# Optimization experiments

Measured on AMD Instinct MI355X. Metric: run time of the kernel, lower is better.

Reference implementation:

```python
import jax, jax.numpy as jnp
import numpy as np

N, E, DIN, HID, DOUT = 50000, 800000, 128, 128, 64
NEG_SLOPE = 0.2


def setup_inputs() -> dict:
    key = jax.random.key(0)
    ks = jax.random.split(key, 16)
    x = jax.random.normal(ks[0], (N, DIN), dtype=jnp.float32)
    edge_index = jax.random.randint(ks[1], (2, E), 0, N, dtype=jnp.int64)

    def lin(k, fan_in, fan_out):
        kw, kb = jax.random.split(k)
        s = 1.0 / np.sqrt(fan_in)
        W = jax.random.uniform(kw, (fan_in, fan_out), jnp.float32, -s, s)
        b = jax.random.uniform(kb, (fan_out,), jnp.float32, -s, s)
        return W, b

    Wl, bl = lin(ks[2], DIN, DIN)   # GATv2 lin_l
    Wr, br = lin(ks[3], DIN, DIN)   # GATv2 lin_r
    att = jax.random.uniform(ks[4], (DIN,), jnp.float32, -1.0 / np.sqrt(DIN), 1.0 / np.sqrt(DIN))
    bg = jnp.zeros((DIN,), jnp.float32)  # GAT output bias
    W1, b1 = lin(ks[5], DIN, HID)   # ChebConv K=1 -> plain linear
    W2, b2 = lin(ks[6], HID, HID)
    W3, b3 = lin(ks[7], HID, DOUT)
    return {"x": x, "edge_index": edge_index, "Wl": Wl, "bl": bl, "Wr": Wr,
            "br": br, "att": att, "bg": bg, "W1": W1, "b1": b1,
            "W2": W2, "b2": b2, "W3": W3, "b3": b3}


def reference(x, edge_index, Wl, bl, Wr, br, att, bg, W1, b1, W2, b2, W3, b3):
    n = x.shape[0]
    # GATv2Conv adds self loops by default
    loop = jnp.arange(n, dtype=edge_index.dtype)
    src = jnp.concatenate([edge_index[0], loop])  # source j
    dst = jnp.concatenate([edge_index[1], loop])  # target i

    xl = x @ Wl + bl  # [N, DIN]
    xr = x @ Wr + br  # [N, DIN]

    # GATv2 edge scores: leaky_relu(x_l[j] + x_r[i]) . att
    e = jax.nn.leaky_relu(xl[src] + xr[dst], NEG_SLOPE)  # [E+N, DIN]
    a = e @ att                                          # [E+N]

    # softmax over incoming edges of each destination node
    amax = jax.ops.segment_max(a, dst, num_segments=n)
    ea = jnp.exp(a - amax[dst])
    denom = jax.ops.segment_sum(ea, dst, num_segments=n)
    alpha = ea / denom[dst]                              # [E+N]

    # aggregate messages alpha * x_l[j] at destinations
    h = jax.ops.segment_sum(alpha[:, None] * xl[src], dst, num_segments=n) + bg

    # ChebConv with K=1 reduces to a linear layer (T_0(L) = I)
    h = jax.nn.relu(h @ W1 + b1)
    h = jax.nn.relu(h @ W2 + b2)
    # dropout_rate = 0.0 -> identity
    return h @ W3 + b3
```

## Files before the change

### kernel.cpp

```cpp
#include <hip/hip_runtime.h>
#include <hip/hip_bf16.h>

#define DIN 128
#define NEG_SLOPE 0.2f
#define PTILE 4096
#define PAD 64
#define SPAD 4608
#define CVT_BLKS 289

typedef __attribute__((ext_vector_type(8))) short bf16x8;
typedef __attribute__((ext_vector_type(8))) unsigned short u16x8;
typedef __attribute__((ext_vector_type(4))) float f32x4;
typedef __attribute__((ext_vector_type(2))) float f32x2;
typedef __attribute__((ext_vector_type(4))) unsigned int u32x4;

__device__ __forceinline__ ushort f2bf(float f) {
  unsigned u = __float_as_uint(f);
  u += 0x7FFFu + ((u >> 16) & 1u);
  return (ushort)(u >> 16);
}
__device__ __forceinline__ f32x2 bfpair(unsigned u) {
  f32x2 r;
  r.x = __uint_as_float(u << 16);
  r.y = __uint_as_float(u & 0xFFFF0000u);
  return r;
}

template <int CTRL>
__device__ __forceinline__ float dppadd(float x) {
  int v = __builtin_amdgcn_update_dpp(0, __float_as_int(x), CTRL, 0xf, 0xf, true);
  return x + __int_as_float(v);
}
__device__ __forceinline__ float red16(float t) {
  t = dppadd<0xB1>(t);
  t = dppadd<0x4E>(t);
  t = dppadd<0x141>(t);
  t = dppadd<0x140>(t);
  return t;
}

__global__ __launch_bounds__(256) void part_cvt_kernel(
    const int* __restrict__ ei, unsigned* __restrict__ part,
    int* __restrict__ cnt2, int ntile, int E,
    const float* __restrict__ Wl, const float* __restrict__ Wr,
    const float* __restrict__ W1, const float* __restrict__ W2,
    const float* __restrict__ W3,
    ushort* __restrict__ WlT, ushort* __restrict__ WrT,
    ushort* __restrict__ W1T, ushort* __restrict__ W2T,
    ushort* __restrict__ W3T) {
  if ((int)blockIdx.x < ntile) {
    __shared__ int hist[256], pref[256], sexcl[256], curs[256];
    __shared__ unsigned buf[PTILE];
    const int tid = threadIdx.x;
    const int t = blockIdx.x;
    const int tile0 = t * PTILE;
    const int tcount = min(PTILE, E - tile0);
    hist[tid] = 0;
    __syncthreads();
    unsigned pk[PTILE / 256];
    int cnt = 0;
    for (int i = tid; i < tcount; i += 256) {
      int s = ei[tile0 + i], d = ei[E + tile0 + i];
      unsigned p = ((unsigned)d << 16) | (unsigned)s;
      pk[cnt++] = p;
      atomicAdd(&hist[d >> 8], 1);
    }
    __syncthreads();
    int v = hist[tid];
    pref[tid] = v;
    __syncthreads();
    for (int d = 1; d < 256; d <<= 1) {
      int tt = (tid >= d) ? pref[tid - d] : 0;
      __syncthreads();
      pref[tid] += tt;
      __syncthreads();
    }
    int exc = pref[tid] - v;
    sexcl[tid] = exc;
    curs[tid] = exc;
    cnt2[tid * ntile + t] = v;
    __syncthreads();
    for (int j = 0; j < cnt; j++) {
      int b = pk[j] >> 24;
      int pos = atomicAdd(&curs[b], 1);
      buf[pos] = pk[j];
    }
    __syncthreads();
    for (int i = tid; i < tcount; i += 256) {
      unsigned p = buf[i];
      int b = p >> 24;
      int r = i - sexcl[b];
      if (r < PAD)
        part[((long)b * ntile + t) * PAD + r] = p;
    }
  } else {
    int i = ((int)blockIdx.x - ntile) * 256 + threadIdx.x;
    if (i < 16384) {
      int k = i >> 7, c = i & 127; WlT[c * 128 + k] = f2bf(Wl[i]);
    } else if (i < 32768) {
      int j = i - 16384; int k = j >> 7, c = j & 127; WrT[c * 128 + k] = f2bf(Wr[j]);
    } else if (i < 49152) {
      int j = i - 32768; int k = j >> 7, c = j & 127; W1T[c * 128 + k] = f2bf(W1[j]);
    } else if (i < 65536) {
      int j = i - 49152; int k = j >> 7, c = j & 127; W2T[c * 128 + k] = f2bf(W2[j]);
    } else if (i < 73728) {
      int j = i - 65536; int k = j >> 6, c = j & 63; W3T[c * 128 + k] = f2bf(W3[j]);
    }
  }
}

__global__ __launch_bounds__(1024) void lin_fine_kernel(
    const float* __restrict__ x,
    const ushort* __restrict__ WlT, const float* __restrict__ bl,
    const ushort* __restrict__ WrT, const float* __restrict__ br,
    ushort* __restrict__ xl, ushort* __restrict__ xr, int n, int nblk_gemm,
    const unsigned* __restrict__ part, const int* __restrict__ cnt2,
    int* __restrict__ offsets, ushort* __restrict__ ecnt,
    ushort* __restrict__ ssrc, int ntile, int N) {
  if ((int)blockIdx.x < nblk_gemm) {
    const int tid1 = threadIdx.x;
    const int sub = tid1 >> 8, tid = tid1 & 255;
    const int wv = tid >> 6, lane = tid & 63;
    const int m = lane & 15, quad = lane >> 4;
    const int colbase = (wv & 1) * 64;
    const int nodew = blockIdx.x * 128 + sub * 32 + (wv >> 1) * 16;
    int arow = nodew + m; if (arow >= n) arow = n - 1;
    f32x4 accl[4], accr[4];
#pragma unroll
    for (int nt = 0; nt < 4; nt++) { accl[nt] = (f32x4){0,0,0,0}; accr[nt] = (f32x4){0,0,0,0}; }
#pragma unroll
    for (int kk = 0; kk < 4; kk++) {
      int k0 = kk * 32 + quad * 8;
      const float4* xp = (const float4*)(x + (long)arow * 128 + k0);
      float4 x0 = xp[0], x1 = xp[1];
      bf16x8 af;
      af[0] = (short)f2bf(x0.x); af[1] = (short)f2bf(x0.y);
      af[2] = (short)f2bf(x0.z); af[3] = (short)f2bf(x0.w);
      af[4] = (short)f2bf(x1.x); af[5] = (short)f2bf(x1.y);
      af[6] = (short)f2bf(x1.z); af[7] = (short)f2bf(x1.w);
#pragma unroll
      for (int nt = 0; nt < 4; nt++) {
        int brow = colbase + nt * 16 + m;
        bf16x8 bl8 = *(const bf16x8*)(WlT + brow * 128 + k0);
        bf16x8 br8 = *(const bf16x8*)(WrT + brow * 128 + k0);
        accl[nt] = __builtin_amdgcn_mfma_f32_16x16x32_bf16(af, bl8, accl[nt], 0, 0, 0);
        accr[nt] = __builtin_amdgcn_mfma_f32_16x16x32_bf16(af, br8, accr[nt], 0, 0, 0);
      }
    }
#pragma unroll
    for (int nt = 0; nt < 4; nt++) {
      int col = colbase + nt * 16 + m;
      float vbl = bl[col], vbr = br[col];
#pragma unroll
      for (int r = 0; r < 4; r++) {
        int node = nodew + quad * 4 + r;
        if (node < n) {
          xl[(long)node * 128 + col] = f2bf(accl[nt][r] + vbl);
          xr[(long)node * 128 + col] = f2bf(accr[nt][r] + vbr);
        }
      }
    }
  } else {
    __shared__ int cnt2s[256], hist[256], curs[256];
    const int tid = threadIdx.x;
    const int b = (int)blockIdx.x - nblk_gemm;
    if (tid < 256) {
      hist[tid] = 0;
      cnt2s[tid] = (tid < ntile) ? cnt2[b * ntile + tid] : 0;
    }
    __syncthreads();
    const long base = (long)b * ntile * PAD;
    const int nv = ntile * PAD;
    for (int v = tid; v < nv; v += 1024) {
      int t = v >> 6;
      if ((v & 63) < cnt2s[t]) {
        unsigned p = part[base + v];
        atomicAdd(&hist[(p >> 16) & 255], 1);
      }
    }
    __syncthreads();
    int v0 = (tid < 256) ? hist[tid] : 0;
    if (tid < 256) curs[tid] = v0;
    __syncthreads();
    for (int d = 1; d < 256; d <<= 1) {
      int tt = (tid >= d && tid < 256) ? curs[tid - d] : 0;
      __syncthreads();
      if (tid < 256) curs[tid] += tt;
      __syncthreads();
    }
    if (tid < 256) {
      int excl = curs[tid] - v0;
      int node = b * 256 + tid;
      if (node < N) {
        offsets[node] = b * SPAD + excl;
        ecnt[node] = (ushort)v0;
      }
      curs[tid] = b * SPAD + excl;
    }
    __syncthreads();
    for (int v = tid; v < nv; v += 1024) {
      int t = v >> 6;
      if ((v & 63) < cnt2s[t]) {
        unsigned p = part[base + v];
        int pos = atomicAdd(&curs[(p >> 16) & 255], 1);
        ssrc[pos] = (ushort)(p & 0xFFFFu);
      }
    }
  }
}

__global__ __launch_bounds__(256) void node_aggr_kernel(
    const ushort* __restrict__ xl, const ushort* __restrict__ xr,
    const float* __restrict__ att, const float* __restrict__ bg,
    const int* __restrict__ offsets, const ushort* __restrict__ ecnt,
    const ushort* __restrict__ ssrc, ushort* __restrict__ h, int n) {
  int wave = (int)((blockIdx.x * (long)blockDim.x + threadIdx.x) >> 6);
  int lane = threadIdx.x & 63;
  if (wave >= n) return;
  const int node = wave;
  const int eg = lane >> 4, sl = lane & 15;
  const int beg = offsets[node];
  const int end = beg + (int)ecnt[node];
  const int last = end - 1;
  const ushort* __restrict__ xls = xl + sl * 8;
  int ia0 = beg + 2 * eg;
  int sa  = (int)ssrc[min(ia0, last)];
  int sb  = (int)ssrc[min(ia0 + 1, last)];
  int sa2 = (int)ssrc[min(ia0 + 8, last)];
  int sb2 = (int)ssrc[min(ia0 + 9, last)];
  u32x4 uva = *(const u32x4*)(xls + (long)sa * 128);
  u32x4 uvb = *(const u32x4*)(xls + (long)sb * 128);

  f32x2 a06[4], a04[4], r2[4], acc2[4];
  {
    const float4* ap = (const float4*)(att + sl * 8);
    float4 a0 = ap[0], a1 = ap[1];
    f32x2 av[4] = {{a0.x, a0.y}, {a0.z, a0.w}, {a1.x, a1.y}, {a1.z, a1.w}};
#pragma unroll
    for (int jp = 0; jp < 4; jp++) {
      a06[jp] = 0.6f * av[jp];
      a04[jp] = 0.4f * av[jp];
    }
  }
  u32x4 rv = *(const u32x4*)(xr + (long)node * 128 + sl * 8);
  u32x4 lv = *(const u32x4*)(xls + (long)node * 128);
  float denom;
  {
    f32x2 t1 = {0.f, 0.f}, t2 = {0.f, 0.f};
    f32x2 l2[4];
#pragma unroll
    for (int jp = 0; jp < 4; jp++) {
      r2[jp] = bfpair(rv[jp]);
      l2[jp] = bfpair(lv[jp]);
      f32x2 v = l2[jp] + r2[jp];
      t1 += a06[jp] * v;
      t2 += a04[jp] * __builtin_elementwise_abs(v);
    }
    float t = red16(t1.x + t1.y + t2.x + t2.y);
    float es = __expf(t);
    denom = (eg == 0) ? es : 0.f;
#pragma unroll
    for (int jp = 0; jp < 4; jp++)
      acc2[jp] = (eg == 0) ? es * l2[jp] : (f32x2){0.f, 0.f};
  }
  for (int p = beg; p < end; p += 8) {
    u32x4 ca = uva, cb = uvb;
    int ia = p + 2 * eg;
    bool cva = ia < end, cvb = ia + 1 < end;
    uva = *(const u32x4*)(xls + (long)sa2 * 128);
    uvb = *(const u32x4*)(xls + (long)sb2 * 128);
    int ian = p + 16 + 2 * eg;
    sa2 = (int)ssrc[min(ian, last)];
    sb2 = (int)ssrc[min(ian + 1, last)];
    f32x2 ua2[4], ub2[4];
    f32x2 ta1 = {0.f, 0.f}, ta2 = {0.f, 0.f};
    f32x2 tb1 = {0.f, 0.f}, tb2 = {0.f, 0.f};
#pragma unroll
    for (int jp = 0; jp < 4; jp++) {
      ua2[jp] = bfpair(ca[jp]);
      ub2[jp] = bfpair(cb[jp]);
      f32x2 va2 = ua2[jp] + r2[jp];
      f32x2 vb2 = ub2[jp] + r2[jp];
      ta1 += a06[jp] * va2;
      ta2 += a04[jp] * __builtin_elementwise_abs(va2);
      tb1 += a06[jp] * vb2;
      tb2 += a04[jp] * __builtin_elementwise_abs(vb2);
    }
    float ta = red16(ta1.x + ta1.y + ta2.x + ta2.y);
    float tb = red16(tb1.x + tb1.y + tb2.x + tb2.y);
    float ea = cva ? __expf(ta) : 0.f;
    float eb = cvb ? __expf(tb) : 0.f;
    denom += ea + eb;
#pragma unroll
    for (int jp = 0; jp < 4; jp++)
      acc2[jp] += ea * ua2[jp] + eb * ub2[jp];
  }
#pragma unroll
  for (int jp = 0; jp < 4; jp++) {
    acc2[jp].x += __shfl_xor(acc2[jp].x, 16);
    acc2[jp].y += __shfl_xor(acc2[jp].y, 16);
    acc2[jp].x += __shfl_xor(acc2[jp].x, 32);
    acc2[jp].y += __shfl_xor(acc2[jp].y, 32);
  }
  denom += __shfl_xor(denom, 16);
  denom += __shfl_xor(denom, 32);
  if (eg == 0) {
    float inv = 1.0f / denom;
    const float4* bp = (const float4*)(bg + sl * 8);
    float4 g0 = bp[0], g1 = bp[1];
    f32x2 gv[4] = {{g0.x, g0.y}, {g0.z, g0.w}, {g1.x, g1.y}, {g1.z, g1.w}};
    u16x8 o;
#pragma unroll
    for (int jp = 0; jp < 4; jp++) {
      f32x2 hv = acc2[jp] * inv + gv[jp];
      o[2 * jp]     = f2bf(hv.x);
      o[2 * jp + 1] = f2bf(hv.y);
    }
    *(u16x8*)(h + (long)node * 128 + sl * 8) = o;
  }
}

#define LDSP 136
__global__ __launch_bounds__(256) void mlp_mfma_kernel(
    const ushort* __restrict__ hb,
    const ushort* __restrict__ W1T, const float* __restrict__ b1,
    const ushort* __restrict__ W2T, const float* __restrict__ b2,
    const ushort* __restrict__ W3T, const float* __restrict__ b3,
    float* __restrict__ out, int n) {
  __shared__ ushort act[32][LDSP];
  const int tid = threadIdx.x;
  const int wv = tid >> 6, lane = tid & 63;
  const int m = lane & 15, quad = lane >> 4;
  const int half = wv & 1, ng = wv >> 1;
  const int colbase = half * 64;
  const int nodew = blockIdx.x * 32 + ng * 16;
  int arow = nodew + m; if (arow >= n) arow = n - 1;
  f32x4 acc[4];
#pragma unroll
  for (int nt = 0; nt < 4; nt++) acc[nt] = (f32x4){0,0,0,0};
#pragma unroll
  for (int kk = 0; kk < 4; kk++) {
    int k0 = kk * 32 + quad * 8;
    bf16x8 af = *(const bf16x8*)(hb + (long)arow * 128 + k0);
#pragma unroll
    for (int nt = 0; nt < 4; nt++) {
      bf16x8 b8 = *(const bf16x8*)(W1T + (colbase + nt * 16 + m) * 128 + k0);
      acc[nt] = __builtin_amdgcn_mfma_f32_16x16x32_bf16(af, b8, acc[nt], 0, 0, 0);
    }
  }
#pragma unroll
  for (int nt = 0; nt < 4; nt++) {
    int col = colbase + nt * 16 + m;
    float b = b1[col];
#pragma unroll
    for (int r = 0; r < 4; r++)
      act[ng * 16 + quad * 4 + r][col] = f2bf(fmaxf(acc[nt][r] + b, 0.f));
  }
  __syncthreads();
#pragma unroll
  for (int nt = 0; nt < 4; nt++) acc[nt] = (f32x4){0,0,0,0};
#pragma unroll
  for (int kk = 0; kk < 4; kk++) {
    int k0 = kk * 32 + quad * 8;
    bf16x8 af = *(const bf16x8*)(&act[ng * 16 + m][k0]);
#pragma unroll
    for (int nt = 0; nt < 4; nt++) {
      bf16x8 b8 = *(const bf16x8*)(W2T + (colbase + nt * 16 + m) * 128 + k0);
      acc[nt] = __builtin_amdgcn_mfma_f32_16x16x32_bf16(af, b8, acc[nt], 0, 0, 0);
    }
  }
  __syncthreads();
#pragma unroll
  for (int nt = 0; nt < 4; nt++) {
    int col = colbase + nt * 16 + m;
    float b = b2[col];
#pragma unroll
    for (int r = 0; r < 4; r++)
      act[ng * 16 + quad * 4 + r][col] = f2bf(fmaxf(acc[nt][r] + b, 0.f));
  }
  __syncthreads();
  f32x4 acc3[2];
#pragma unroll
  for (int nt = 0; nt < 2; nt++) acc3[nt] = (f32x4){0,0,0,0};
#pragma unroll
  for (int kk = 0; kk < 4; kk++) {
    int k0 = kk * 32 + quad * 8;
    bf16x8 af = *(const bf16x8*)(&act[ng * 16 + m][k0]);
#pragma unroll
    for (int nt = 0; nt < 2; nt++) {
      bf16x8 b8 = *(const bf16x8*)(W3T + (half * 32 + nt * 16 + m) * 128 + k0);
      acc3[nt] = __builtin_amdgcn_mfma_f32_16x16x32_bf16(af, b8, acc3[nt], 0, 0, 0);
    }
  }
#pragma unroll
  for (int nt = 0; nt < 2; nt++) {
    int col = half * 32 + nt * 16 + m;
    float b = b3[col];
#pragma unroll
    for (int r = 0; r < 4; r++) {
      int node = nodew + quad * 4 + r;
      if (node < n) out[(long)node * 64 + col] = acc3[nt][r] + b;
    }
  }
}

extern "C" void kernel_launch(void* const* d_in, const int* in_sizes, int n_in,
                              void* d_out, int out_size, void* d_ws, size_t ws_size,
                              hipStream_t stream) {
  const float* x   = (const float*)d_in[0];
  const int*   ei  = (const int*)d_in[1];
  const float* Wl  = (const float*)d_in[2];
  const float* bl  = (const float*)d_in[3];
  const float* Wr  = (const float*)d_in[4];
  const float* br  = (const float*)d_in[5];
  const float* att = (const float*)d_in[6];
  const float* bg  = (const float*)d_in[7];
  const float* W1  = (const float*)d_in[8];
  const float* b1  = (const float*)d_in[9];
  const float* W2  = (const float*)d_in[10];
  const float* b2  = (const float*)d_in[11];
  const float* W3  = (const float*)d_in[12];
  const float* b3  = (const float*)d_in[13];
  float* out = (float*)d_out;

  const int N = in_sizes[0] / DIN;
  const int E = in_sizes[1] / 2;
  const int nbuck = (N + 255) >> 8;
  const int ntile = (E + PTILE - 1) / PTILE;

  char* ws = (char*)d_ws;
  size_t off = 0;
  auto alloc = [&](size_t bytes) {
    void* p = ws + off;
    off += (bytes + 255) & ~(size_t)255;
    return p;
  };
  int* cnt2      = (int*)alloc((size_t)256 * ntile * 4);
  int* offsets   = (int*)alloc(((size_t)N + 4) * 4);
  ushort* ecnt   = (ushort*)alloc(((size_t)N + 16) * 2);
  ushort* ssrc   = (ushort*)alloc((size_t)256 * SPAD * 2 + 256);
  ushort* xlb    = (ushort*)alloc((size_t)N * DIN * 2);
  ushort* xrb    = (ushort*)alloc((size_t)N * DIN * 2);
  size_t part_bytes = (size_t)256 * ntile * PAD * 4;
  size_t hbf_bytes  = (size_t)N * DIN * 2;
  unsigned* part = (unsigned*)alloc(part_bytes > hbf_bytes ? part_bytes : hbf_bytes);
  ushort* hbf    = (ushort*)part;
  ushort* WlT    = (ushort*)alloc(16384 * 2);
  ushort* WrT    = (ushort*)alloc(16384 * 2);
  ushort* W1T    = (ushort*)alloc(16384 * 2);
  ushort* W2T    = (ushort*)alloc(16384 * 2);
  ushort* W3T    = (ushort*)alloc(8192 * 2);
  (void)ws_size;

  part_cvt_kernel<<<ntile + CVT_BLKS, 256, 0, stream>>>(
      ei, part, cnt2, ntile, E,
      Wl, Wr, W1, W2, W3, WlT, WrT, W1T, W2T, W3T);

  int nblk_gemm = (N + 127) / 128;
  lin_fine_kernel<<<nblk_gemm + nbuck, 1024, 0, stream>>>(
      x, WlT, bl, WrT, br, xlb, xrb, N, nblk_gemm,
      part, cnt2, offsets, ecnt, ssrc, ntile, N);

  int nwblk = (N + 3) / 4;
  node_aggr_kernel<<<nwblk, 256, 0, stream>>>(xlb, xrb, att, bg,
                                              offsets, ecnt, ssrc, hbf, N);

  int nblk32 = (N + 31) / 32;
  mlp_mfma_kernel<<<nblk32, 256, 0, stream>>>(hbf, W1T, b1, W2T, b2,
                                              W3T, b3, out, N);
}
```

Before: 237.6 us.

## Precompute per-node attention dot products and stage GEMM tiles through LDS

Splits leaky_relu as 0.6*v + 0.4*|v|, so the linear term's dot with att becomes per-node scalars al and ar. These are computed in the GEMM epilogue and added per edge, removing half the per-edge FMA work in aggregation at the cost of one extra scalar load per edge. The GEMM now stages the bf16 x tile and the outputs through shared memory for coalesced 16-byte loads and stores, and the MLP kernel stages its h input tile in LDS as well. These add synchronisation barriers and LDS usage.

```diff
diff --git a/kernel.cpp b/kernel.cpp
--- a/kernel.cpp
+++ b/kernel.cpp
@@ -18,6 +18,9 @@
   unsigned u = __float_as_uint(f);
   u += 0x7FFFu + ((u >> 16) & 1u);
   return (ushort)(u >> 16);
+}
+__device__ __forceinline__ float bf2f(ushort u) {
+  return __uint_as_float((unsigned)u << 16);
 }
 __device__ __forceinline__ f32x2 bfpair(unsigned u) {
   f32x2 r;
@@ -109,35 +112,46 @@
   }
 }
 
+#define XSP 136
 __global__ __launch_bounds__(1024) void lin_fine_kernel(
-    const float* __restrict__ x,
+    const float* __restrict__ x, const float* __restrict__ att,
     const ushort* __restrict__ WlT, const float* __restrict__ bl,
     const ushort* __restrict__ WrT, const float* __restrict__ br,
-    ushort* __restrict__ xl, ushort* __restrict__ xr, int n, int nblk_gemm,
+    ushort* __restrict__ xl, ushort* __restrict__ xr,
+    float* __restrict__ al, float* __restrict__ ar, int n, int nblk_gemm,
     const unsigned* __restrict__ part, const int* __restrict__ cnt2,
     int* __restrict__ offsets, ushort* __restrict__ ecnt,
     ushort* __restrict__ ssrc, int ntile, int N) {
   if ((int)blockIdx.x < nblk_gemm) {
+    __shared__ ushort xs[4][32][XSP];
     const int tid1 = threadIdx.x;
     const int sub = tid1 >> 8, tid = tid1 & 255;
     const int wv = tid >> 6, lane = tid & 63;
     const int m = lane & 15, quad = lane >> 4;
     const int colbase = (wv & 1) * 64;
-    const int nodew = blockIdx.x * 128 + sub * 32 + (wv >> 1) * 16;
-    int arow = nodew + m; if (arow >= n) arow = n - 1;
+    const int ng = wv >> 1;
+    const int nodew0 = blockIdx.x * 128 + sub * 32;
+    const int srow = tid >> 3, scol = (tid & 7) * 16;
+    {
+      int grow = nodew0 + srow; if (grow >= n) grow = n - 1;
+      const float4* xp = (const float4*)(x + (long)grow * 128 + scol);
+      float4 f0 = xp[0], f1 = xp[1], f2 = xp[2], f3 = xp[3];
+      u16x8 o0, o1;
+      o0[0] = f2bf(f0.x); o0[1] = f2bf(f0.y); o0[2] = f2bf(f0.z); o0[3] = f2bf(f0.w);
+      o0[4] = f2bf(f1.x); o0[5] = f2bf(f1.y); o0[6] = f2bf(f1.z); o0[7] = f2bf(f1.w);
+      o1[0] = f2bf(f2.x); o1[1] = f2bf(f2.y); o1[2] = f2bf(f2.z); o1[3] = f2bf(f2.w);
+      o1[4] = f2bf(f3.x); o1[5] = f2bf(f3.y); o1[6] = f2bf(f3.z); o1[7] = f2bf(f3.w);
+      *(u16x8*)&xs[sub][srow][scol]     = o0;
+      *(u16x8*)&xs[sub][srow][scol + 8] = o1;
+    }
+    __syncthreads();
     f32x4 accl[4], accr[4];
 #pragma unroll
     for (int nt = 0; nt < 4; nt++) { accl[nt] = (f32x4){0,0,0,0}; accr[nt] = (f32x4){0,0,0,0}; }
 #pragma unroll
     for (int kk = 0; kk < 4; kk++) {
       int k0 = kk * 32 + quad * 8;
-      const float4* xp = (const float4*)(x + (long)arow * 128 + k0);
-      float4 x0 = xp[0], x1 = xp[1];
-      bf16x8 af;
-      af[0] = (short)f2bf(x0.x); af[1] = (short)f2bf(x0.y);
-      af[2] = (short)f2bf(x0.z); af[3] = (short)f2bf(x0.w);
-      af[4] = (short)f2bf(x1.x); af[5] = (short)f2bf(x1.y);
-      af[6] = (short)f2bf(x1.z); af[7] = (short)f2bf(x1.w);
+      bf16x8 af = *(const bf16x8*)&xs[sub][ng * 16 + m][k0];
 #pragma unroll
       for (int nt = 0; nt < 4; nt++) {
         int brow = colbase + nt * 16 + m;
@@ -147,18 +161,59 @@
         accr[nt] = __builtin_amdgcn_mfma_f32_16x16x32_bf16(af, br8, accr[nt], 0, 0, 0);
       }
     }
+    __syncthreads();
 #pragma unroll
     for (int nt = 0; nt < 4; nt++) {
       int col = colbase + nt * 16 + m;
-      float vbl = bl[col], vbr = br[col];
-#pragma unroll
-      for (int r = 0; r < 4; r++) {
-        int node = nodew + quad * 4 + r;
-        if (node < n) {
-          xl[(long)node * 128 + col] = f2bf(accl[nt][r] + vbl);
-          xr[(long)node * 128 + col] = f2bf(accr[nt][r] + vbr);
-        }
+      float vb = bl[col];
+#pragma unroll
+      for (int r = 0; r < 4; r++)
+        xs[sub][ng * 16 + quad * 4 + r][col] = f2bf(accl[nt][r] + vb);
+    }
+    __syncthreads();
+    {
+      int node = nodew0 + srow;
+      u16x8 o0 = *(u16x8*)&xs[sub][srow][scol];
+      u16x8 o1 = *(u16x8*)&xs[sub][srow][scol + 8];
+      if (node < n) {
+        *(u16x8*)(xl + (long)node * 128 + scol)     = o0;
+        *(u16x8*)(xl + (long)node * 128 + scol + 8) = o1;
       }
+      const float4* ap = (const float4*)(att + scol);
+      float4 a0 = ap[0], a1 = ap[1], a2 = ap[2], a3 = ap[3];
+      float ps = a0.x*bf2f(o0[0]) + a0.y*bf2f(o0[1]) + a0.z*bf2f(o0[2]) + a0.w*bf2f(o0[3])
+               + a1.x*bf2f(o0[4]) + a1.y*bf2f(o0[5]) + a1.z*bf2f(o0[6]) + a1.w*bf2f(o0[7])
+               + a2.x*bf2f(o1[0]) + a2.y*bf2f(o1[1]) + a2.z*bf2f(o1[2]) + a2.w*bf2f(o1[3])
+               + a3.x*bf2f(o1[4]) + a3.y*bf2f(o1[5]) + a3.z*bf2f(o1[6]) + a3.w*bf2f(o1[7]);
+      ps += __shfl_xor(ps, 1); ps += __shfl_xor(ps, 2); ps += __shfl_xor(ps, 4);
+      if ((tid & 7) == 0 && node < n) al[node] = ps;
+    }
+    __syncthreads();
+#pragma unroll
+    for (int nt = 0; nt < 4; nt++) {
+      int col = colbase + nt * 16 + m;
+      float vb = br[col];
+#pragma unroll
+      for (int r = 0; r < 4; r++)
+        xs[sub][ng * 16 + quad * 4 + r][col] = f2bf(accr[nt][r] + vb);
+    }
+    __syncthreads();
+    {
+      int node = nodew0 + srow;
+      u16x8 o0 = *(u16x8*)&xs[sub][srow][scol];
+      u16x8 o1 = *(u16x8*)&xs[sub][srow][scol + 8];
+      if (node < n) {
+        *(u16x8*)(xr + (long)node * 128 + scol)     = o0;
+        *(u16x8*)(xr + (long)node * 128 + scol + 8) = o1;
+      }
+      const float4* ap = (const float4*)(att + scol);
+      float4 a0 = ap[0], a1 = ap[1], a2 = ap[2], a3 = ap[3];
+      float ps = a0.x*bf2f(o0[0]) + a0.y*bf2f(o0[1]) + a0.z*bf2f(o0[2]) + a0.w*bf2f(o0[3])
+               + a1.x*bf2f(o0[4]) + a1.y*bf2f(o0[5]) + a1.z*bf2f(o0[6]) + a1.w*bf2f(o0[7])
+               + a2.x*bf2f(o1[0]) + a2.y*bf2f(o1[1]) + a2.z*bf2f(o1[2]) + a2.w*bf2f(o1[3])
+               + a3.x*bf2f(o1[4]) + a3.y*bf2f(o1[5]) + a3.z*bf2f(o1[6]) + a3.w*bf2f(o1[7]);
+      ps += __shfl_xor(ps, 1); ps += __shfl_xor(ps, 2); ps += __shfl_xor(ps, 4);
+      if ((tid & 7) == 0 && node < n) ar[node] = ps;
     }
   } else {
     __shared__ int cnt2s[256], hist[256], curs[256];
@@ -212,6 +267,7 @@
 __global__ __launch_bounds__(256) void node_aggr_kernel(
     const ushort* __restrict__ xl, const ushort* __restrict__ xr,
     const float* __restrict__ att, const float* __restrict__ bg,
+    const float* __restrict__ al, const float* __restrict__ ar,
     const int* __restrict__ offsets, const ushort* __restrict__ ecnt,
     const ushort* __restrict__ ssrc, ushort* __restrict__ h, int n) {
   int wave = (int)((blockIdx.x * (long)blockDim.x + threadIdx.x) >> 6);
@@ -230,33 +286,31 @@
   int sb2 = (int)ssrc[min(ia0 + 9, last)];
   u32x4 uva = *(const u32x4*)(xls + (long)sa * 128);
   u32x4 uvb = *(const u32x4*)(xls + (long)sb * 128);
-
-  f32x2 a06[4], a04[4], r2[4], acc2[4];
+  float ala = al[sa], alb = al[sb];
+  const float arn = ar[node];
+
+  f32x2 a04[4], r2[4], acc2[4];
   {
     const float4* ap = (const float4*)(att + sl * 8);
     float4 a0 = ap[0], a1 = ap[1];
     f32x2 av[4] = {{a0.x, a0.y}, {a0.z, a0.w}, {a1.x, a1.y}, {a1.z, a1.w}};
 #pragma unroll
-    for (int jp = 0; jp < 4; jp++) {
-      a06[jp] = 0.6f * av[jp];
-      a04[jp] = 0.4f * av[jp];
-    }
+    for (int jp = 0; jp < 4; jp++) a04[jp] = 0.4f * av[jp];
   }
   u32x4 rv = *(const u32x4*)(xr + (long)node * 128 + sl * 8);
   u32x4 lv = *(const u32x4*)(xls + (long)node * 128);
   float denom;
   {
-    f32x2 t1 = {0.f, 0.f}, t2 = {0.f, 0.f};
+    f32x2 t2 = {0.f, 0.f};
     f32x2 l2[4];
 #pragma unroll
     for (int jp = 0; jp < 4; jp++) {
       r2[jp] = bfpair(rv[jp]);
       l2[jp] = bfpair(lv[jp]);
       f32x2 v = l2[jp] + r2[jp];
-      t1 += a06[jp] * v;
       t2 += a04[jp] * __builtin_elementwise_abs(v);
     }
-    float t = red16(t1.x + t1.y + t2.x + t2.y);
+    float t = red16(t2.x + t2.y) + 0.6f * (al[node] + arn);
     float es = __expf(t);
     denom = (eg == 0) ? es : 0.f;
 #pragma unroll
@@ -265,29 +319,28 @@
   }
   for (int p = beg; p < end; p += 8) {
     u32x4 ca = uva, cb = uvb;
+    float cala = ala, calb = alb;
     int ia = p + 2 * eg;
     bool cva = ia < end, cvb = ia + 1 < end;
     uva = *(const u32x4*)(xls + (long)sa2 * 128);
     uvb = *(const u32x4*)(xls + (long)sb2 * 128);
+    ala = al[sa2]; alb = al[sb2];
     int ian = p + 16 + 2 * eg;
     sa2 = (int)ssrc[min(ian, last)];
     sb2 = (int)ssrc[min(ian + 1, last)];
     f32x2 ua2[4], ub2[4];
-    f32x2 ta1 = {0.f, 0.f}, ta2 = {0.f, 0.f};
-    f32x2 tb1 = {0.f, 0.f}, tb2 = {0.f, 0.f};
+    f32x2 ta2 = {0.f, 0.f}, tb2 = {0.f, 0.f};
 #pragma unroll
     for (int jp = 0; jp < 4; jp++) {
       ua2[jp] = bfpair(ca[jp]);
       ub2[jp] = bfpair(cb[jp]);
       f32x2 va2 = ua2[jp] + r2[jp];
       f32x2 vb2 = ub2[jp] + r2[jp];
-      ta1 += a06[jp] * va2;
       ta2 += a04[jp] * __builtin_elementwise_abs(va2);
-      tb1 += a06[jp] * vb2;
       tb2 += a04[jp] * __builtin_elementwise_abs(vb2);
     }
-    float ta = red16(ta1.x + ta1.y + ta2.x + ta2.y);
-    float tb = red16(tb1.x + tb1.y + tb2.x + tb2.y);
+    float ta = red16(ta2.x + ta2.y) + 0.6f * (cala + arn);
+    float tb = red16(tb2.x + tb2.y) + 0.6f * (calb + arn);
     float ea = cva ? __expf(ta) : 0.f;
     float eb = cvb ? __expf(tb) : 0.f;
     denom += ea + eb;
@@ -327,6 +380,7 @@
     const ushort* __restrict__ W2T, const float* __restrict__ b2,
     const ushort* __restrict__ W3T, const float* __restrict__ b3,
     float* __restrict__ out, int n) {
+  __shared__ ushort hst[32][LDSP];
   __shared__ ushort act[32][LDSP];
   const int tid = threadIdx.x;
   const int wv = tid >> 6, lane = tid & 63;
@@ -334,14 +388,22 @@
   const int half = wv & 1, ng = wv >> 1;
   const int colbase = half * 64;
   const int nodew = blockIdx.x * 32 + ng * 16;
-  int arow = nodew + m; if (arow >= n) arow = n - 1;
+  {
+    const int srow = tid >> 3, scol = (tid & 7) * 16;
+    int grow = blockIdx.x * 32 + srow; if (grow >= n) grow = n - 1;
+    u16x8 o0 = *(const u16x8*)(hb + (long)grow * 128 + scol);
+    u16x8 o1 = *(const u16x8*)(hb + (long)grow * 128 + scol + 8);
+    *(u16x8*)&hst[srow][scol]     = o0;
+    *(u16x8*)&hst[srow][scol + 8] = o1;
+  }
+  __syncthreads();
   f32x4 acc[4];
 #pragma unroll
   for (int nt = 0; nt < 4; nt++) acc[nt] = (f32x4){0,0,0,0};
 #pragma unroll
   for (int kk = 0; kk < 4; kk++) {
     int k0 = kk * 32 + quad * 8;
-    bf16x8 af = *(const bf16x8*)(hb + (long)arow * 128 + k0);
+    bf16x8 af = *(const bf16x8*)(&hst[ng * 16 + m][k0]);
 #pragma unroll
     for (int nt = 0; nt < 4; nt++) {
       bf16x8 b8 = *(const bf16x8*)(W1T + (colbase + nt * 16 + m) * 128 + k0);
@@ -441,6 +503,8 @@
   ushort* ssrc   = (ushort*)alloc((size_t)256 * SPAD * 2 + 256);
   ushort* xlb    = (ushort*)alloc((size_t)N * DIN * 2);
   ushort* xrb    = (ushort*)alloc((size_t)N * DIN * 2);
+  float* albuf   = (float*)alloc((size_t)N * 4);
+  float* arbuf   = (float*)alloc((size_t)N * 4);
   size_t part_bytes = (size_t)256 * ntile * PAD * 4;
   size_t hbf_bytes  = (size_t)N * DIN * 2;
   unsigned* part = (unsigned*)alloc(part_bytes > hbf_bytes ? part_bytes : hbf_bytes);
@@ -458,11 +522,12 @@
 
   int nblk_gemm = (N + 127) / 128;
   lin_fine_kernel<<<nblk_gemm + nbuck, 1024, 0, stream>>>(
-      x, WlT, bl, WrT, br, xlb, xrb, N, nblk_gemm,
+      x, att, WlT, bl, WrT, br, xlb, xrb, albuf, arbuf, N, nblk_gemm,
       part, cnt2, offsets, ecnt, ssrc, ntile, N);
 
   int nwblk = (N + 3) / 4;
   node_aggr_kernel<<<nwblk, 256, 0, stream>>>(xlb, xrb, att, bg,
+                                              albuf, arbuf,
                                               offsets, ecnt, ssrc, hbf, N);
 
   int nblk32 = (N + 31) / 32;
```

Result: no change. 234.9 us (-1.1%).
